# Kernel optimization log

Measured on AMD Instinct MI355X. Metric: run time of the kernel, lower is better.

The kernel has to match this reference:

```python
import jax, jax.numpy as jnp
import numpy as np

EPS = 1e-5


def _extract3x3(x, stride=1):
    # channel-major patch extraction: output [B, C*9, Ho, Wo], each channel's 3x3 window contiguous
    B, C, H, W = x.shape
    xp = jnp.pad(x, ((0, 0), (0, 0), (1, 1), (1, 1)))
    Ho = (H + 2 - 3) // stride + 1
    Wo = (W + 2 - 3) // stride + 1
    pats = [xp[:, :, i:i + (Ho - 1) * stride + 1:stride, j:j + (Wo - 1) * stride + 1:stride]
            for i in range(3) for j in range(3)]
    return jnp.stack(pats, axis=2).reshape(B, C * 9, Ho, Wo)


def _amm(patches, centroids, lut, inv_temp):
    # patches: [B, D, H, W] channel-major, D = ncodebooks * subvec_len
    # centroids: [ncb, k, sub], lut: [ncb, k, out_channels]
    B, D, H, W = patches.shape
    ncb, k, sub = centroids.shape
    v = patches.reshape(B, ncb, sub, H * W).transpose(0, 3, 1, 2)  # [B, L, ncb, sub]
    # negative squared distance to each codeword (||v||^2 dropped: constant over k)
    scores = 2.0 * jnp.einsum('blcs,cks->blck', v, centroids) - jnp.sum(centroids * centroids, -1)[None, None]
    attn = jax.nn.softmax(scores * inv_temp, axis=-1)          # soft codeword assignment
    out = jnp.einsum('blck,cko->blo', attn, lut)                # LUT gather/sum over codebooks
    return out.transpose(0, 2, 1).reshape(B, -1, H, W)


def _bn(x, g, b):
    m = x.mean((0, 2, 3), keepdims=True)
    v = x.var((0, 2, 3), keepdims=True)
    return g[None, :, None, None] * (x - m) * jax.lax.rsqrt(v + EPS) + b[None, :, None, None]


def setup_inputs() -> dict:
    key = jax.random.key(0)
    ks = jax.random.split(key, 8)
    B, C, H, W = 32, 1024, 14, 14
    width, out_c, K = 256, 1024, 16
    return {
        'x': jax.random.normal(ks[0], (B, C, H, W), jnp.float32),
        'c1_centroids': jax.random.normal(ks[1], (C // 4, K, 4), jnp.float32),
        'c1_lut': jax.random.normal(ks[2], (C // 4, K, width), jnp.float32) * 0.05,
        'c1_invt': jnp.ones((), jnp.float32),
        'c2_centroids': jax.random.normal(ks[3], (width, K, 9), jnp.float32),
        'c2_lut': jax.random.normal(ks[4], (width, K, width), jnp.float32) * 0.05,
        'c2_invt': jnp.ones((), jnp.float32),
        'c3_centroids': jax.random.normal(ks[5], (width // 4, K, 4), jnp.float32),
        'c3_lut': jax.random.normal(ks[6], (width // 4, K, out_c), jnp.float32) * 0.05,
        'c3_invt': jnp.ones((), jnp.float32),
        'bn1_g': jnp.ones((width,), jnp.float32), 'bn1_b': jnp.zeros((width,), jnp.float32),
        'bn2_g': jnp.ones((width,), jnp.float32), 'bn2_b': jnp.zeros((width,), jnp.float32),
        'bn3_g': jnp.ones((out_c,), jnp.float32), 'bn3_b': jnp.zeros((out_c,), jnp.float32),
    }


def reference(x, c1_centroids, c1_lut, c1_invt, c2_centroids, c2_lut, c2_invt,
              c3_centroids, c3_lut, c3_invt, bn1_g, bn1_b, bn2_g, bn2_b, bn3_g, bn3_b):
    identity = x
    out = _amm(x, c1_centroids, c1_lut, c1_invt)                 # amm_conv1x1, stride 1
    out = jax.nn.relu(_bn(out, bn1_g, bn1_b))
    out = _amm(_extract3x3(out, 1), c2_centroids, c2_lut, c2_invt)  # amm_conv3x3, stride 1, pad 1
    out = jax.nn.relu(_bn(out, bn2_g, bn2_b))
    out = _amm(out, c3_centroids, c3_lut, c3_invt)               # amm_conv1x1
    out = _bn(out, bn3_g, bn3_b)
    return jax.nn.relu(out + identity)
```

## Files before the change

### kernel.cpp

```cpp
#include <hip/hip_runtime.h>
#include <hip/hip_bf16.h>

#define EPSV 1e-5f

typedef unsigned short u16;
typedef __attribute__((ext_vector_type(8))) short short8;
typedef __attribute__((ext_vector_type(4))) float f32x4;
typedef __hip_bfloat16 bf16;

__device__ __forceinline__ unsigned int pack2(float a, float b) {
  bf16 ha = __float2bfloat16(a), hb = __float2bfloat16(b);
  u16 ua, ub;
  __builtin_memcpy(&ua, &ha, 2);
  __builtin_memcpy(&ub, &hb, 2);
  return (unsigned int)ua | ((unsigned int)ub << 16);
}

typedef __attribute__((address_space(1))) const void gvoid_t;
typedef __attribute__((address_space(3))) void lvoid_t;
__device__ __forceinline__ void gload16(const void* g, void* l) {
  __builtin_amdgcn_global_load_lds((gvoid_t*)g, (lvoid_t*)l, 16, 0, 0);
}


__global__ __launch_bounds__(256) void prep_kernel(
    const float* __restrict__ x, const float* __restrict__ cent,
    const float* __restrict__ invt, u16* __restrict__ attn,
    const float* __restrict__ s1, bf16* __restrict__ d1,
    const float* __restrict__ s2, bf16* __restrict__ d2,
    const float* __restrict__ s3, bf16* __restrict__ d3)
{
  __shared__ __align__(16) float sh[7012];
  const int tid = threadIdx.x;
  if (blockIdx.x >= 1024) {
    const int bid = blockIdx.x - 1024;
    const int which = bid >> 8, sub = bid & 255;
    const float* in = (which == 0) ? s1 : (which == 1) ? s2 : s3;
    bf16* out = (which == 0) ? d1 : (which == 1) ? d2 : d3;
    const int K = (which == 2) ? 1024 : 4096;
    const int N = (which == 2) ? 1024 : 256;
    const int kt = K >> 6;
    const int bk = sub & (kt - 1), bn = sub / kt;
    const int k0 = bk * 64, n0 = bn * 64;
    float* t = sh;
    for (int idx = tid; idx < 4096; idx += 256) {
      int r = idx >> 6, c = idx & 63;
      t[r * 65 + c] = in[(size_t)(k0 + r) * N + n0 + c];
    }
    __syncthreads();
    for (int idx = tid; idx < 4096; idx += 256) {
      int r = idx >> 6, c = idx & 63;
      out[(size_t)(n0 + r) * K + k0 + c] = __float2bfloat16(t[c * 65 + r]);
    }
    return;
  }
  float* vs = sh;
  float* cs = sh + 6468;
  const int bi = blockIdx.x >> 5, cg = blockIdx.x & 31;
  const float* xb = x + ((size_t)bi * 1024 + cg * 32) * 196;
  for (int e = tid; e < 3136; e += 256) {
    int c = e / 98, p2 = e - c * 98;
    float2 w = *(const float2*)&xb[(size_t)c * 196 + p2 * 2];
    vs[(p2 * 2) * 33 + c] = w.x;
    vs[(p2 * 2 + 1) * 33 + c] = w.y;
  }
  if (tid < 128) {
    int cb = tid >> 4, kk = tid & 15;
    *(float4*)&cs[cb * 68 + kk * 4] =
        *(const float4*)&cent[(size_t)(cg * 8 + cb) * 64 + kk * 4];
  }
  __syncthreads();
  const float it = invt[0];
  const int cbL = tid & 7, pj = tid >> 3;
  float4 cv[16]; float cn[16];
  #pragma unroll
  for (int k = 0; k < 16; k++) {
    cv[k] = *(const float4*)&cs[cbL * 68 + k * 4];
    cn[k] = cv[k].x * cv[k].x + cv[k].y * cv[k].y + cv[k].z * cv[k].z + cv[k].w * cv[k].w;
  }
  for (int p = pj; p < 196; p += 32) {
    const float* vp = &vs[p * 33 + cbL * 4];
    const float v0 = vp[0], v1 = vp[1], v2 = vp[2], v3 = vp[3];
    float s[16], mx = -3e38f;
    #pragma unroll
    for (int k = 0; k < 16; k++) {
      float d = v0 * cv[k].x + v1 * cv[k].y + v2 * cv[k].z + v3 * cv[k].w;
      s[k] = it * (2.f * d - cn[k]);
      mx = fmaxf(mx, s[k]);
    }
    float sum = 0.f;
    #pragma unroll
    for (int k = 0; k < 16; k++) { float e = __expf(s[k] - mx); s[k] = e; sum += e; }
    const float r = 1.f / sum;
    uint4 w0, w1;
    w0.x = pack2(s[0] * r,  s[1] * r);  w0.y = pack2(s[2] * r,  s[3] * r);
    w0.z = pack2(s[4] * r,  s[5] * r);  w0.w = pack2(s[6] * r,  s[7] * r);
    w1.x = pack2(s[8] * r,  s[9] * r);  w1.y = pack2(s[10] * r, s[11] * r);
    w1.z = pack2(s[12] * r, s[13] * r); w1.w = pack2(s[14] * r, s[15] * r);
    uint4* dst = (uint4*)(attn + (size_t)(bi * 196 + p) * 4096 + (cg * 8 + cbL) * 16);
    dst[0] = w0; dst[1] = w1;
  }
}

__global__ __launch_bounds__(256) void attn2_kernel(const float* __restrict__ out1,
    const float* __restrict__ g, const float* __restrict__ bb,
    const float* __restrict__ Sacc, const float* __restrict__ cent,
    const float* __restrict__ invt, u16* __restrict__ attn)
{
  __shared__ float vs[4 * 16 * 32];
  __shared__ __align__(16) float cs[32 * 196];
  __shared__ float ssl[64];
  const int tid = threadIdx.x;
  const int rp = blockIdx.x >> 3, cg = blockIdx.x & 7;
  const int b = rp / 7, y0 = (rp % 7) * 2, m0 = rp * 28;
  if (tid < 32) {
    const int ch = cg * 32 + tid;
    float S = Sacc[ch], S2 = Sacc[256 + ch];
    float mean = S * (1.f / 6272.f);
    float var = S2 * (1.f / 6272.f) - mean * mean;
    float sc = g[ch] * rsqrtf(var + EPSV);
    ssl[tid] = sc; ssl[32 + tid] = bb[ch] - mean * sc;
  }
  __syncthreads();
  for (int e = tid; e < 2048; e += 256) {
    int c = e & 31, x1 = (e >> 5) & 15, dyy = e >> 9;
    int yy = y0 + dyy - 1, xx = x1 - 1;
    float v = 0.f;
    int ch = cg * 32 + c;
    if (yy >= 0 && yy < 14 && xx >= 0 && xx < 14) {
      float val = out1[(size_t)((b * 14 + yy) * 14 + xx) * 256 + ch];
      v = fmaxf(val * ssl[c] + ssl[32 + c], 0.f);
    }
    vs[e] = v;
  }
  for (int idx = tid; idx < 1152; idx += 256) {
    int cb = idx / 36, f4i = idx - cb * 36;
    float4 w = *(const float4*)&cent[(size_t)(cg * 32 + cb) * 144 + f4i * 4];
    int j0 = f4i * 4;
    #pragma unroll
    for (int t = 0; t < 4; t++) {
      int j = j0 + t, k = j / 9, jj = j - k * 9;
      cs[cb * 196 + k * 12 + jj] = ((const float*)&w)[t];
    }
  }
  __syncthreads();
  const float it = invt[0];
  const int cb = tid & 31, pq = tid >> 5;
  const int np = (pq < 4) ? 4 : 3;
  float v[4][9];
  #pragma unroll
  for (int i = 0; i < 4; i++) if (i < np) {
    const int p = i * 8 + pq;
    const int r = p / 14, xc = p - r * 14;
    #pragma unroll
    for (int dy = 0; dy < 3; dy++)
      #pragma unroll
      for (int dx = 0; dx < 3; dx++)
        v[i][dy * 3 + dx] = vs[((r + dy) * 16 + xc + dx) * 32 + cb];
  }
  float s[4][16];
  #pragma unroll
  for (int k = 0; k < 16; k++) {
    const float* ck = &cs[cb * 196 + k * 12];
    const float4 ca = *(const float4*)ck;
    const float4 cbv = *(const float4*)(ck + 4);
    const float c8 = ck[8];
    float c9[9] = {ca.x, ca.y, ca.z, ca.w, cbv.x, cbv.y, cbv.z, cbv.w, c8};
    float cn = 0.f;
    #pragma unroll
    for (int j = 0; j < 9; j++) cn = fmaf(c9[j], c9[j], cn);
    #pragma unroll
    for (int i = 0; i < 4; i++) if (i < np) {
      float d = 0.f;
      #pragma unroll
      for (int j = 0; j < 9; j++) d = fmaf(c9[j], v[i][j], d);
      s[i][k] = it * (2.f * d - cn);
    }
  }
  #pragma unroll
  for (int i = 0; i < 4; i++) if (i < np) {
    float mx = -3e38f;
    #pragma unroll
    for (int k = 0; k < 16; k++) mx = fmaxf(mx, s[i][k]);
    float sum = 0.f;
    #pragma unroll
    for (int k = 0; k < 16; k++) { float e = __expf(s[i][k] - mx); s[i][k] = e; sum += e; }
    const float r = 1.f / sum;
    uint4 w0, w1;
    w0.x = pack2(s[i][0] * r,  s[i][1] * r);  w0.y = pack2(s[i][2] * r,  s[i][3] * r);
    w0.z = pack2(s[i][4] * r,  s[i][5] * r);  w0.w = pack2(s[i][6] * r,  s[i][7] * r);
    w1.x = pack2(s[i][8] * r,  s[i][9] * r);  w1.y = pack2(s[i][10] * r, s[i][11] * r);
    w1.z = pack2(s[i][12] * r, s[i][13] * r); w1.w = pack2(s[i][14] * r, s[i][15] * r);
    uint4* dst = (uint4*)(attn + (size_t)(m0 + i * 8 + pq) * 4096 + (cg * 32 + cb) * 16);
    dst[0] = w0; dst[1] = w1;
  }
}

__global__ __launch_bounds__(256) void attn3_kernel(const float* __restrict__ out2,
    const float* __restrict__ g, const float* __restrict__ bb,
    const float* __restrict__ Sacc, const float* __restrict__ cent,
    const float* __restrict__ invt, bf16* __restrict__ attn)
{
  __shared__ float ssl[512];
  const int t = threadIdx.x;
  {
    float S = Sacc[t], S2 = Sacc[256 + t];
    float mean = S * (1.f / 6272.f);
    float var = S2 * (1.f / 6272.f) - mean * mean;
    float sc = g[t] * rsqrtf(var + EPSV);
    ssl[t] = sc; ssl[256 + t] = bb[t] - mean * sc;
  }
  __syncthreads();
  const int cb = t & 63, ml = t >> 6;
  const int m0 = blockIdx.x * 16;
  const float it = invt[0];
  float4 cv[16]; float cn[16];
  const float4* cc = (const float4*)(cent + cb * 64);
  #pragma unroll
  for (int k = 0; k < 16; k++) {
    cv[k] = cc[k];
    cn[k] = cv[k].x * cv[k].x + cv[k].y * cv[k].y + cv[k].z * cv[k].z + cv[k].w * cv[k].w;
  }
  const float4 scv = *(const float4*)(ssl + cb * 4);
  const float4 shv = *(const float4*)(ssl + 256 + cb * 4);
  for (int gi = 0; gi < 4; gi++) {
    const int m = m0 + gi * 4 + ml;
    float4 xv = *(const float4*)(out2 + (size_t)m * 256 + cb * 4);
    float4 v;
    v.x = fmaxf(xv.x * scv.x + shv.x, 0.f);
    v.y = fmaxf(xv.y * scv.y + shv.y, 0.f);
    v.z = fmaxf(xv.z * scv.z + shv.z, 0.f);
    v.w = fmaxf(xv.w * scv.w + shv.w, 0.f);
    float s[16], mx = -3e38f;
    #pragma unroll
    for (int k = 0; k < 16; k++) {
      float d = v.x * cv[k].x + v.y * cv[k].y + v.z * cv[k].z + v.w * cv[k].w;
      s[k] = it * (2.f * d - cn[k]);
      mx = fmaxf(mx, s[k]);
    }
    float sum = 0.f;
    #pragma unroll
    for (int k = 0; k < 16; k++) { float e = __expf(s[k] - mx); s[k] = e; sum += e; }
    float r = 1.f / sum;
    #pragma unroll
    for (int k = 0; k < 16; k++)
      attn[(size_t)m * 1024 + cb * 16 + k] = __float2bfloat16(s[k] * r);
  }
}

template<int KDIM, int NT, int KSLICES, int BM, int BK>
__global__ __launch_bounds__(256) void gemm_kernel(const u16* __restrict__ A,
    const u16* __restrict__ Bt, float* __restrict__ C, size_t cstride,
    float* __restrict__ zacc, int zn)
{
  constexpr int NDIM = NT * 128;
  constexpr int KS = KDIM / KSLICES;
  constexpr int MT = 6272 / BM;
  constexpr int FM = BM / 32;
  constexpr int KU = BK / 32;
  constexpr int SLOTS = BK / 8;
  constexpr int RPC = 64 / SLOTS;
  constexpr int ACALLS = BM / (RPC * 4);
  constexpr int BCALLS = 128 / (RPC * 4);
  __shared__ __align__(16) u16 Asm[2][BM * BK];
  __shared__ __align__(16) u16 Bsm[2][128 * BK];
  const int tid = threadIdx.x;
  if (blockIdx.x == 0 && zacc) {
    for (int i = tid; i < zn; i += 256) zacc[i] = 0.f;
  }
  const int nwg = gridDim.x;
  int wg = blockIdx.x;
  if ((nwg & 7) == 0) wg = (blockIdx.x & 7) * (nwg >> 3) + (blockIdx.x >> 3);
  const int nt = wg % NT;
  const int mt = (wg / NT) % MT;
  const int sl = wg / (NT * MT);
  const int kbeg = sl * KS, kend = kbeg + KS;
  const int m0 = mt * BM, n0 = nt * 128;
  const int lane = tid & 63, wid = tid >> 6;
  const int wm = wid >> 1, wn = wid & 1;
  const int lr = lane / SLOTS, sslot = lane % SLOTS;
  const int gs = sslot ^ (lr & 7);

  f32x4 acc[FM][4];
  #pragma unroll
  for (int i = 0; i < FM; i++)
    #pragma unroll
    for (int j = 0; j < 4; j++) acc[i][j] = (f32x4){0.f, 0.f, 0.f, 0.f};

  const u16* Abase = A + (size_t)m0 * KDIM;
  const u16* Bbase = Bt + (size_t)n0 * KDIM;

  auto stage = [&](int bf, int kb) {
    #pragma unroll
    for (int c = 0; c < ACALLS; c++) {
      const int r0 = (wid * ACALLS + c) * RPC;
      gload16(Abase + (size_t)(r0 + lr) * KDIM + kb + gs * 8, &Asm[bf][r0 * BK]);
    }
    #pragma unroll
    for (int c = 0; c < BCALLS; c++) {
      const int r0 = (wid * BCALLS + c) * RPC;
      gload16(Bbase + (size_t)(r0 + lr) * KDIM + kb + gs * 8, &Bsm[bf][r0 * BK]);
    }
  };

  auto compute = [&](int bf) {
    #pragma unroll
    for (int ks = 0; ks < KU; ks++) {
      short8 a[FM], b[4];
      #pragma unroll
      for (int f = 0; f < FM; f++) {
        const int ra = wm * (BM / 2) + f * 16 + (lane & 15);
        const int ja = (ks * 4 + (lane >> 4)) ^ (ra & 7);
        a[f] = *(const short8*)(&Asm[bf][ra * BK + ja * 8]);
      }
      #pragma unroll
      for (int f = 0; f < 4; f++) {
        const int rb = wn * 64 + f * 16 + (lane & 15);
        const int jb = (ks * 4 + (lane >> 4)) ^ (rb & 7);
        b[f] = *(const short8*)(&Bsm[bf][rb * BK + jb * 8]);
      }
      #pragma unroll
      for (int fm = 0; fm < FM; fm++)
        #pragma unroll
        for (int fn = 0; fn < 4; fn++)
          acc[fm][fn] = __builtin_amdgcn_mfma_f32_16x16x32_bf16(a[fm], b[fn], acc[fm][fn], 0, 0, 0);
    }
  };

  stage(0, kbeg);
  __syncthreads();
  int cur = 0;
  for (int kb = kbeg + BK; kb < kend; kb += BK) {
    stage(cur ^ 1, kb);
    compute(cur);
    __syncthreads();
    cur ^= 1;
  }
  compute(cur);

  float* __restrict__ Cs = C + (size_t)sl * cstride;
  #pragma unroll
  for (int fm = 0; fm < FM; fm++)
    #pragma unroll
    for (int fn = 0; fn < 4; fn++) {
      const int col = n0 + wn * 64 + fn * 16 + (lane & 15);
      const int rbase = m0 + wm * (BM / 2) + fm * 16 + (lane >> 4) * 4;
      #pragma unroll
      for (int r = 0; r < 4; r++)
        Cs[(size_t)(rbase + r) * NDIM + col] = acc[fm][fn][r];
    }
}

template<int CH, int NBLK, int NSUM>
__global__ __launch_bounds__(256) void bnpart_kernel(const float* __restrict__ buf,
    float* __restrict__ sum_out, float* __restrict__ acc)
{
  constexpr int PC = CH / 256;
  constexpr int ROWS = 6272 / NBLK;
  constexpr size_t PSTR = 6272ull * CH;
  const int t = threadIdx.x, m0 = blockIdx.x * ROWS;
  float s[PC], s2[PC];
  #pragma unroll
  for (int j = 0; j < PC; j++) { s[j] = 0.f; s2[j] = 0.f; }
  for (int i = 0; i < ROWS; i++) {
    const size_t ro = (size_t)(m0 + i) * CH;
    #pragma unroll
    for (int j = 0; j < PC; j++) {
      float v = buf[ro + t + j * 256];
      #pragma unroll
      for (int n = 1; n < NSUM; n++) v += buf[(size_t)n * PSTR + ro + t + j * 256];
      if (NSUM > 1) sum_out[ro + t + j * 256] = v;
      s[j] += v; s2[j] = fmaf(v, v, s2[j]);
    }
  }
  #pragma unroll
  for (int j = 0; j < PC; j++) {
    atomicAdd(&acc[t + j * 256], s[j]);
    atomicAdd(&acc[CH + t + j * 256], s2[j]);
  }
}

__global__ __launch_bounds__(256) void tfinal_kernel(const float* __restrict__ out3,
    const float* __restrict__ g, const float* __restrict__ bb,
    const float* __restrict__ Sacc, const float* __restrict__ x,
    float* __restrict__ out)
{
  __shared__ float t[64 * 199];
  __shared__ float ssl[128];
  const int b = blockIdx.x >> 4, n0 = (blockIdx.x & 15) * 64;
  if (threadIdx.x < 64) {
    const int ch = n0 + threadIdx.x;
    float S = Sacc[ch], S2 = Sacc[1024 + ch];
    float mean = S * (1.f / 6272.f);
    float var = S2 * (1.f / 6272.f) - mean * mean;
    float sc = g[ch] * rsqrtf(var + EPSV);
    ssl[threadIdx.x] = sc; ssl[64 + threadIdx.x] = bb[ch] - mean * sc;
  }
  __syncthreads();
  for (int idx = threadIdx.x; idx < 196 * 64; idx += 256) {
    int p = idx >> 6, ni = idx & 63;
    float v = out3[(size_t)(b * 196 + p) * 1024 + n0 + ni] * ssl[ni] + ssl[64 + ni];
    t[ni * 199 + p] = v;
  }
  __syncthreads();
  for (int idx = threadIdx.x; idx < 64 * 196; idx += 256) {
    int ni = idx / 196, p = idx - ni * 196;
    size_t o = (size_t)(b * 1024 + n0 + ni) * 196 + p;
    out[o] = fmaxf(t[ni * 199 + p] + x[o], 0.f);
  }
}


template<int CIN, int OUT, bool APPLY_BN>
__global__ __launch_bounds__(256) void amm1x1_kernel(
    const float* __restrict__ xin, const float* __restrict__ ss,
    const float* __restrict__ cent, const float* __restrict__ lut,
    const float* __restrict__ invt, float* __restrict__ outbuf)
{
  constexpr int NCB = CIN / 4;
  constexpr int NO = OUT / 256;
  __shared__ float vsm[CIN * 14];
  __shared__ __align__(16) float attn_sm[14 * 16];
  const int tid = threadIdx.x;
  const int b = blockIdx.x / 14, y = blockIdx.x % 14;
  const int rowbase = y * 14;
  for (int e = tid; e < CIN * 14; e += 256) {
    int c = e / 14, xc = e - c * 14;
    float v = xin[(b * CIN + c) * 196 + rowbase + xc];
    if (APPLY_BN) v = fmaxf(v * ss[c] + ss[CIN + c], 0.f);
    vsm[e] = v;
  }
  __syncthreads();
  float acc[14 * NO];
  #pragma unroll
  for (int i = 0; i < 14 * NO; i++) acc[i] = 0.f;
  const float it = invt[0];
  const int p_ = tid >> 4, k_ = tid & 15;
  for (int cb = 0; cb < NCB; ++cb) {
    if (tid < 224) {
      const float* cc = cent + (cb * 16 + k_) * 4;
      float s = 0.f;
      #pragma unroll
      for (int si = 0; si < 4; si++) {
        float cv = cc[si];
        float vv = vsm[(cb * 4 + si) * 14 + p_];
        s = fmaf(cv, 2.f * vv - cv, s);
      }
      s *= it;
      float m = s;
      #pragma unroll
      for (int off = 8; off; off >>= 1) m = fmaxf(m, __shfl_xor(m, off, 16));
      float e = __expf(s - m);
      float sum = e;
      #pragma unroll
      for (int off = 8; off; off >>= 1) sum += __shfl_xor(sum, off, 16);
      attn_sm[p_ * 16 + k_] = e / sum;
    }
    __syncthreads();
    float lv[NO][16];
    #pragma unroll
    for (int j = 0; j < NO; j++)
      #pragma unroll
      for (int k = 0; k < 16; k++)
        lv[j][k] = lut[(cb * 16 + k) * OUT + j * 256 + tid];
    const float4* a4 = (const float4*)attn_sm;
    #pragma unroll
    for (int p = 0; p < 14; p++) {
      float4 q0 = a4[p*4+0], q1 = a4[p*4+1], q2 = a4[p*4+2], q3 = a4[p*4+3];
      float av[16] = {q0.x,q0.y,q0.z,q0.w, q1.x,q1.y,q1.z,q1.w,
                      q2.x,q2.y,q2.z,q2.w, q3.x,q3.y,q3.z,q3.w};
      #pragma unroll
      for (int j = 0; j < NO; j++) {
        float s = acc[p * NO + j];
        #pragma unroll
        for (int k = 0; k < 16; k++) s = fmaf(av[k], lv[j][k], s);
        acc[p * NO + j] = s;
      }
    }
    __syncthreads();
  }
  #pragma unroll
  for (int j = 0; j < NO; j++) {
    int o = j * 256 + tid;
    #pragma unroll
    for (int p = 0; p < 14; p++)
      outbuf[(b * OUT + o) * 196 + rowbase + p] = acc[p * NO + j];
  }
}

__global__ __launch_bounds__(256) void amm3x3_kernel(
    const float* __restrict__ xin, const float* __restrict__ ss,
    const float* __restrict__ cent, const float* __restrict__ lut,
    const float* __restrict__ invt, float* __restrict__ outbuf)
{
  __shared__ float vsm[256 * 3 * 16];
  __shared__ __align__(16) float attn_sm[14 * 16];
  const int tid = threadIdx.x;
  const int b = blockIdx.x / 14, y = blockIdx.x % 14;
  for (int e = tid; e < 256 * 3 * 16; e += 256) {
    int c = e / 48, rem = e - c * 48, i = rem >> 4, col = rem & 15;
    int yy = y + i - 1, xx = col - 1;
    float v = 0.f;
    if (yy >= 0 && yy < 14 && xx >= 0 && xx < 14) {
      v = xin[(b * 256 + c) * 196 + yy * 14 + xx];
      v = fmaxf(v * ss[c] + ss[256 + c], 0.f);
    }
    vsm[e] = v;
  }
  __syncthreads();
  float acc[14];
  #pragma unroll
  for (int i = 0; i < 14; i++) acc[i] = 0.f;
  const float it = invt[0];
  const int p_ = tid >> 4, k_ = tid & 15;
  for (int cb = 0; cb < 256; ++cb) {
    if (tid < 224) {
      const float* cc = cent + (cb * 16 + k_) * 9;
      float s = 0.f;
      #pragma unroll
      for (int i = 0; i < 3; i++)
        #pragma unroll
        for (int j = 0; j < 3; j++) {
          float cv = cc[i * 3 + j];
          float vv = vsm[(cb * 3 + i) * 16 + p_ + j];
          s = fmaf(cv, 2.f * vv - cv, s);
        }
      s *= it;
      float m = s;
      #pragma unroll
      for (int off = 8; off; off >>= 1) m = fmaxf(m, __shfl_xor(m, off, 16));
      float e = __expf(s - m);
      float sum = e;
      #pragma unroll
      for (int off = 8; off; off >>= 1) sum += __shfl_xor(sum, off, 16);
      attn_sm[p_ * 16 + k_] = e / sum;
    }
    __syncthreads();
    float lv[16];
    #pragma unroll
    for (int k = 0; k < 16; k++) lv[k] = lut[(cb * 16 + k) * 256 + tid];
    const float4* a4 = (const float4*)attn_sm;
    #pragma unroll
    for (int p = 0; p < 14; p++) {
      float4 q0 = a4[p*4+0], q1 = a4[p*4+1], q2 = a4[p*4+2], q3 = a4[p*4+3];
      float av[16] = {q0.x,q0.y,q0.z,q0.w, q1.x,q1.y,q1.z,q1.w,
                      q2.x,q2.y,q2.z,q2.w, q3.x,q3.y,q3.z,q3.w};
      float s = acc[p];
      #pragma unroll
      for (int k = 0; k < 16; k++) s = fmaf(av[k], lv[k], s);
      acc[p] = s;
    }
    __syncthreads();
  }
  #pragma unroll
  for (int p = 0; p < 14; p++)
    outbuf[(b * 256 + tid) * 196 + y * 14 + p] = acc[p];
}

template<int CH>
__global__ __launch_bounds__(256) void bnstats_kernel(const float* __restrict__ buf,
    const float* __restrict__ g, const float* __restrict__ bb, float* __restrict__ ss)
{
  const int c = blockIdx.x, tid = threadIdx.x;
  float s = 0.f, s2 = 0.f;
  for (int e = tid; e < 32 * 196; e += 256) {
    int bi = e / 196, l = e - bi * 196;
    float v = buf[(bi * CH + c) * 196 + l];
    s += v; s2 = fmaf(v, v, s2);
  }
  #pragma unroll
  for (int off = 32; off; off >>= 1) { s += __shfl_down(s, off); s2 += __shfl_down(s2, off); }
  __shared__ float red[8];
  int w = tid >> 6;
  if ((tid & 63) == 0) { red[w] = s; red[4 + w] = s2; }
  __syncthreads();
  if (tid == 0) {
    float S  = red[0] + red[1] + red[2] + red[3];
    float S2 = red[4] + red[5] + red[6] + red[7];
    float mean = S * (1.f / 6272.f);
    float var  = S2 * (1.f / 6272.f) - mean * mean;
    float sc = g[c] * rsqrtf(var + EPSV);
    ss[c] = sc;
    ss[CH + c] = bb[c] - mean * sc;
  }
}

__global__ __launch_bounds__(256) void final_old_kernel(float* __restrict__ out3,
    const float* __restrict__ ss, const float* __restrict__ x)
{
  const int total = 32 * 1024 * 196;
  for (int idx = blockIdx.x * 256 + threadIdx.x; idx < total; idx += gridDim.x * 256) {
    int c = (idx / 196) & 1023;
    float v = out3[idx] * ss[c] + ss[1024 + c] + x[idx];
    out3[idx] = fmaxf(v, 0.f);
  }
}


extern "C" void kernel_launch(void* const* d_in, const int* in_sizes, int n_in,
                              void* d_out, int out_size, void* d_ws, size_t ws_size,
                              hipStream_t stream) {
  const float* x   = (const float*)d_in[0];
  const float* c1c = (const float*)d_in[1];
  const float* c1l = (const float*)d_in[2];
  const float* c1t = (const float*)d_in[3];
  const float* c2c = (const float*)d_in[4];
  const float* c2l = (const float*)d_in[5];
  const float* c2t = (const float*)d_in[6];
  const float* c3c = (const float*)d_in[7];
  const float* c3l = (const float*)d_in[8];
  const float* c3t = (const float*)d_in[9];
  const float* g1  = (const float*)d_in[10];
  const float* b1  = (const float*)d_in[11];
  const float* g2  = (const float*)d_in[12];
  const float* b2  = (const float*)d_in[13];
  const float* g3  = (const float*)d_in[14];
  const float* b3  = (const float*)d_in[15];

  float* ws = (float*)d_ws;
  const size_t FAST_NEED = 24255488ull * 4ull;

  if (ws_size >= FAST_NEED) {
    u16*   attnB = (u16*)ws;
    float* partC = ws + 12845056;
    float* out1  = partC + 6422528;
    float* out2  = out1 + 1605632;
    bf16*  lutT1 = (bf16*)(out2 + 1605632);
    bf16*  lutT2 = lutT1 + 1048576;
    bf16*  lutT3 = lutT2 + 1048576;
    float* acc1  = (float*)(lutT3 + 1048576);
    float* acc2  = acc1 + 512;
    float* acc3  = acc2 + 512;
    float* out3  = partC;
    const size_t PART_STRIDE = 1605632;

    prep_kernel<<<1792, 256, 0, stream>>>(x, c1c, c1t, attnB,
                                          c1l, lutT1, c2l, lutT2, c3l, lutT3);

    gemm_kernel<4096, 2, 4, 128, 64><<<392, 256, 0, stream>>>(
        attnB, (const u16*)lutT1, partC, PART_STRIDE, acc1, 512);
    bnpart_kernel<256, 196, 4><<<196, 256, 0, stream>>>(partC, out1, acc1);

    attn2_kernel<<<1792, 256, 0, stream>>>(out1, g1, b1, acc1, c2c, c2t, attnB);
    gemm_kernel<4096, 2, 4, 128, 64><<<392, 256, 0, stream>>>(
        attnB, (const u16*)lutT2, partC, PART_STRIDE, acc2, 512);
    bnpart_kernel<256, 196, 4><<<196, 256, 0, stream>>>(partC, out2, acc2);

    attn3_kernel<<<392, 256, 0, stream>>>(out2, g2, b2, acc2, c3c, c3t, (bf16*)attnB);
    gemm_kernel<1024, 8, 1, 128, 64><<<392, 256, 0, stream>>>(
        attnB, (const u16*)lutT3, out3, 0, acc3, 2048);
    bnpart_kernel<1024, 98, 1><<<98, 256, 0, stream>>>(out3, nullptr, acc3);

    tfinal_kernel<<<512, 256, 0, stream>>>(out3, g3, b3, acc3, x, (float*)d_out);
  } else {
    float* out3 = (float*)d_out;
    float* out1 = ws;
    float* out2 = out1 + 32 * 256 * 196;
    float* ss1  = out2 + 32 * 256 * 196;
    float* ss2  = ss1 + 512;
    float* ss3  = ss2 + 512;

    amm1x1_kernel<1024, 256, false><<<448, 256, 0, stream>>>(x, nullptr, c1c, c1l, c1t, out1);
    bnstats_kernel<256><<<256, 256, 0, stream>>>(out1, g1, b1, ss1);
    amm3x3_kernel<<<448, 256, 0, stream>>>(out1, ss1, c2c, c2l, c2t, out2);
    bnstats_kernel<256><<<256, 256, 0, stream>>>(out2, g2, b2, ss2);
    amm1x1_kernel<256, 1024, true><<<448, 256, 0, stream>>>(out2, ss2, c3c, c3l, c3t, out3);
    bnstats_kernel<1024><<<1024, 256, 0, stream>>>(out3, g3, b3, ss3);
    final_old_kernel<<<2048, 256, 0, stream>>>(out3, ss3, x);
  }
}
```

Baseline: 292.2 us.

## Fuse third-layer BN statistics into GEMM epilogue and precompute centroid norms

The third GEMM now reduces per-column sums and sums of squares from its accumulators in registers and shared memory, then atomically adds them into the stats buffer. This removes the separate bnpart pass that re-read the full 6272x1024 output. Zeroing of that stats buffer moves into the second GEMM launch. In attn2, centroids are pre-scaled by 2/T and their squared norms are computed once into shared memory, which trims per-score arithmetic. The cost is float atomics and a slightly different summation order for the statistics.

```diff
diff --git a/kernel.cpp b/kernel.cpp
--- a/kernel.cpp
+++ b/kernel.cpp
@@ -109,10 +109,12 @@
 {
   __shared__ float vs[4 * 16 * 32];
   __shared__ __align__(16) float cs[32 * 196];
+  __shared__ float cnl[32 * 17];
   __shared__ float ssl[64];
   const int tid = threadIdx.x;
   const int rp = blockIdx.x >> 3, cg = blockIdx.x & 7;
   const int b = rp / 7, y0 = (rp % 7) * 2, m0 = rp * 28;
+  const float it = invt[0];
   if (tid < 32) {
     const int ch = cg * 32 + tid;
     float S = Sacc[ch], S2 = Sacc[256 + ch];
@@ -133,6 +135,7 @@
     }
     vs[e] = v;
   }
+  const float it2 = 2.f * it;
   for (int idx = tid; idx < 1152; idx += 256) {
     int cb = idx / 36, f4i = idx - cb * 36;
     float4 w = *(const float4*)&cent[(size_t)(cg * 32 + cb) * 144 + f4i * 4];
@@ -140,11 +143,18 @@
     #pragma unroll
     for (int t = 0; t < 4; t++) {
       int j = j0 + t, k = j / 9, jj = j - k * 9;
-      cs[cb * 196 + k * 12 + jj] = ((const float*)&w)[t];
-    }
-  }
-  __syncthreads();
-  const float it = invt[0];
+      cs[cb * 196 + k * 12 + jj] = it2 * ((const float*)&w)[t];
+    }
+  }
+  for (int idx = tid; idx < 512; idx += 256) {
+    int cb = idx >> 4, k = idx & 15;
+    const float* cc = &cent[(size_t)(cg * 32 + cb) * 144 + k * 9];
+    float cn = 0.f;
+    #pragma unroll
+    for (int j = 0; j < 9; j++) cn = fmaf(cc[j], cc[j], cn);
+    cnl[cb * 17 + k] = it * cn;
+  }
+  __syncthreads();
   const int cb = tid & 31, pq = tid >> 5;
   const int np = (pq < 4) ? 4 : 3;
   float v[4][9];
@@ -165,16 +175,14 @@
     const float4 ca = *(const float4*)ck;
     const float4 cbv = *(const float4*)(ck + 4);
     const float c8 = ck[8];
+    const float cnv = cnl[cb * 17 + k];
     float c9[9] = {ca.x, ca.y, ca.z, ca.w, cbv.x, cbv.y, cbv.z, cbv.w, c8};
-    float cn = 0.f;
-    #pragma unroll
-    for (int j = 0; j < 9; j++) cn = fmaf(c9[j], c9[j], cn);
     #pragma unroll
     for (int i = 0; i < 4; i++) if (i < np) {
-      float d = 0.f;
+      float d = -cnv;
       #pragma unroll
       for (int j = 0; j < 9; j++) d = fmaf(c9[j], v[i][j], d);
-      s[i][k] = it * (2.f * d - cn);
+      s[i][k] = d;
     }
   }
   #pragma unroll
@@ -251,7 +259,7 @@
 template<int KDIM, int NT, int KSLICES, int BM, int BK>
 __global__ __launch_bounds__(256) void gemm_kernel(const u16* __restrict__ A,
     const u16* __restrict__ Bt, float* __restrict__ C, size_t cstride,
-    float* __restrict__ zacc, int zn)
+    float* __restrict__ zacc, int zn, float* __restrict__ stats)
 {
   constexpr int NDIM = NT * 128;
   constexpr int KS = KDIM / KSLICES;
@@ -349,6 +357,33 @@
       for (int r = 0; r < 4; r++)
         Cs[(size_t)(rbase + r) * NDIM + col] = acc[fm][fn][r];
     }
+
+  if (stats) {
+    __syncthreads();
+    float* red = (float*)&Asm[0][0];
+    #pragma unroll
+    for (int fn = 0; fn < 4; fn++) {
+      float s = 0.f, s2 = 0.f;
+      #pragma unroll
+      for (int fm = 0; fm < FM; fm++)
+        #pragma unroll
+        for (int r = 0; r < 4; r++) {
+          float v = acc[fm][fn][r];
+          s += v; s2 = fmaf(v, v, s2);
+        }
+      s += __shfl_xor(s, 16);  s += __shfl_xor(s, 32);
+      s2 += __shfl_xor(s2, 16); s2 += __shfl_xor(s2, 32);
+      if ((lane >> 4) == 0) {
+        const int colL = wn * 64 + fn * 16 + (lane & 15);
+        red[wm * 256 + colL] = s;
+        red[wm * 256 + 128 + colL] = s2;
+      }
+    }
+    __syncthreads();
+    const int colL = tid & 127, st = (tid >> 7) & 1;
+    float v = red[st * 128 + colL] + red[256 + st * 128 + colL];
+    atomicAdd(&stats[(size_t)st * NDIM + n0 + colL], v);
+  }
 }
 
 template<int CH, int NBLK, int NSUM>
@@ -638,18 +673,17 @@
                                           c1l, lutT1, c2l, lutT2, c3l, lutT3);
 
     gemm_kernel<4096, 2, 4, 128, 64><<<392, 256, 0, stream>>>(
-        attnB, (const u16*)lutT1, partC, PART_STRIDE, acc1, 512);
+        attnB, (const u16*)lutT1, partC, PART_STRIDE, acc1, 512, nullptr);
     bnpart_kernel<256, 196, 4><<<196, 256, 0, stream>>>(partC, out1, acc1);
 
     attn2_kernel<<<1792, 256, 0, stream>>>(out1, g1, b1, acc1, c2c, c2t, attnB);
     gemm_kernel<4096, 2, 4, 128, 64><<<392, 256, 0, stream>>>(
-        attnB, (const u16*)lutT2, partC, PART_STRIDE, acc2, 512);
+        attnB, (const u16*)lutT2, partC, PART_STRIDE, acc2, 2560, nullptr);
     bnpart_kernel<256, 196, 4><<<196, 256, 0, stream>>>(partC, out2, acc2);
 
     attn3_kernel<<<392, 256, 0, stream>>>(out2, g2, b2, acc2, c3c, c3t, (bf16*)attnB);
     gemm_kernel<1024, 8, 1, 128, 64><<<392, 256, 0, stream>>>(
-        attnB, (const u16*)lutT3, out3, 0, acc3, 2048);
-    bnpart_kernel<1024, 98, 1><<<98, 256, 0, stream>>>(out3, nullptr, acc3);
+        attnB, (const u16*)lutT3, out3, 0, nullptr, 0, acc3);
 
     tfinal_kernel<<<512, 256, 0, stream>>>(out3, g3, b3, acc3, x, (float*)d_out);
   } else {
```

Result: no change. 286.6 us (-1.9%).
